# Performance work log

Measured on AMD Instinct MI355X. Metric: run time of the kernel, lower is better.

The kernel has to match this reference:

```python
import jax, jax.numpy as jnp
import numpy as np

N_NODES = 50000


def _graph_conv(x, edges, W0, b0, W1, b1):
    # Symmetric (undirected) message passing: each edge (a,b) sends x[b]->a and x[a]->b.
    src = jnp.concatenate([edges[:, 0], edges[:, 1]])  # [2E]
    dst = jnp.concatenate([edges[:, 1], edges[:, 0]])  # [2E]
    deg = jax.ops.segment_sum(jnp.ones_like(dst, dtype=x.dtype), dst, num_segments=N_NODES)
    deg = jnp.maximum(deg, 1.0)  # avoid div-by-zero for isolated nodes
    agg = jax.ops.segment_sum(x[src], dst, num_segments=N_NODES) / deg[:, None]  # [N, F]
    # self transform + normalized-neighbor transform
    return x @ W0 + b0 + agg @ W1 + b1


def setup_inputs() -> dict:
    key = jax.random.key(0)
    ks = jax.random.split(key, 10)
    feats = [256, 512, 256]  # [in] + hidden + [out]
    inp = {
        "vert_features": jax.random.normal(ks[0], (N_NODES, feats[0]), dtype=jnp.float32),
        "edges": jax.random.randint(ks[1], (400000, 2), 0, N_NODES, dtype=jnp.int64),
    }
    kidx = 2
    for l, (fi, fo) in enumerate(zip(feats[:-1], feats[1:])):
        s = 1.0 / np.sqrt(fi)
        inp[f"W0_{l}"] = jax.random.normal(ks[kidx], (fi, fo), dtype=jnp.float32) * s
        inp[f"b0_{l}"] = jnp.zeros((fo,), dtype=jnp.float32)
        inp[f"W1_{l}"] = jax.random.normal(ks[kidx + 1], (fi, fo), dtype=jnp.float32) * s
        inp[f"b1_{l}"] = jnp.zeros((fo,), dtype=jnp.float32)
        kidx += 2
    return inp


def reference(vert_features, edges, W0_0, b0_0, W1_0, b1_0, W0_1, b0_1, W1_1, b1_1):
    # layer 0 + ReLU
    x = _graph_conv(vert_features, edges, W0_0, b0_0, W1_0, b1_0)
    x = jax.nn.relu(x)
    # final layer (no activation)
    x = _graph_conv(x, edges, W0_1, b0_1, W1_1, b1_1)
    return x
```

## Files before the change

### kernel.cpp

```cpp
#include <hip/hip_runtime.h>
#include <stdint.h>

typedef __bf16  bf16x8 __attribute__((ext_vector_type(8)));
typedef float   f32x4  __attribute__((ext_vector_type(4)));

__device__ __forceinline__ unsigned short f2bf(float f) {
  unsigned int u = __float_as_uint(f);
  u += 0x7fffu + ((u >> 16) & 1u);
  return (unsigned short)(u >> 16);
}
__device__ __forceinline__ float bflo(unsigned int v) { return __uint_as_float(v << 16); }
__device__ __forceinline__ float bfhi(unsigned int v) { return __uint_as_float(v & 0xffff0000u); }

__global__ void detect_fmt_kernel(const int* __restrict__ eg, int* __restrict__ fmt) {
  if (threadIdx.x == 0 && blockIdx.x == 0) {
    int is64 = 1;
    for (int i = 1; i < 32; i += 2) if (eg[i] != 0) { is64 = 0; break; }
    fmt[0] = is64;
  }
}

__global__ void phase1_kernel(const float* __restrict__ x, unsigned short* __restrict__ A0, int n,
                              const int* __restrict__ eg, const int* __restrict__ fmt,
                              int* __restrict__ deg, int E,
                              const float* __restrict__ W00, const float* __restrict__ W10,
                              const float* __restrict__ W01, const float* __restrict__ W11,
                              const float* __restrict__ b00, const float* __restrict__ b10,
                              const float* __restrict__ b01, const float* __restrict__ b11,
                              unsigned short* __restrict__ Bt1, unsigned short* __restrict__ Bt2,
                              float* __restrict__ bias1, float* __restrict__ bias2) {
  const int i = blockIdx.x * 256 + threadIdx.x;
  if (i < n * 64) {
    const int row = i >> 6, c4 = i & 63;
    const float4 v = ((const float4*)x)[i];
    ushort4 o;
    o.x = f2bf(v.x); o.y = f2bf(v.y); o.z = f2bf(v.z); o.w = f2bf(v.w);
    *(ushort4*)&A0[(size_t)row * 512 + c4 * 4] = o;
  }
  if (i < 512 * 512) {
    const int nn = i >> 9, k = i & 511;
    const float v1 = (k < 256) ? W00[k * 512 + nn] : W10[(k - 256) * 512 + nn];
    Bt1[i] = f2bf(v1);
    const float v2 = (nn < 256) ? W01[k * 256 + nn] : W11[k * 256 + (nn - 256)];
    Bt2[i] = f2bf(v2);
    if (i < 512) {
      bias1[i] = b00[i] + b10[i];
      bias2[i] = (i < 256) ? (b01[i] + b11[i]) : 0.f;
    }
  }
  if (i < E) {
    int a, b;
    if (fmt[0]) { a = eg[4 * i]; b = eg[4 * i + 2]; }
    else        { a = eg[2 * i]; b = eg[2 * i + 1]; }
    if ((unsigned)a < (unsigned)n && (unsigned)b < (unsigned)n) {
      atomicAdd(&deg[a], 1);
      atomicAdd(&deg[b], 1);
    }
  }
}

__global__ void block_sum_kernel(const int* __restrict__ deg, int* __restrict__ bsum, int n) {
  const int t = threadIdx.x;
  const int i = blockIdx.x * 1024 + t;
  int v = (i < n) ? deg[i] : 0;
  #pragma unroll
  for (int d = 32; d > 0; d >>= 1) v += __shfl_xor(v, d);
  __shared__ int ws[16];
  if ((t & 63) == 0) ws[t >> 6] = v;
  __syncthreads();
  if (t < 16) {
    int s = ws[t];
    #pragma unroll
    for (int d = 1; d < 16; d <<= 1) s += __shfl_xor(s, d);
    if (t == 0) bsum[blockIdx.x] = s;
  }
}

__global__ void scan_bsum_kernel(int* __restrict__ bsum, int* __restrict__ off, int nb, int n) {
  const int l = threadIdx.x;
  int v = (l < nb) ? bsum[l] : 0;
  const int orig = v;
  #pragma unroll
  for (int d = 1; d < 64; d <<= 1) {
    int u = __shfl_up(v, d);
    if (l >= d) v += u;
  }
  if (l < nb) bsum[l] = v - orig;
  if (l == nb - 1) off[n] = v;
}

__global__ void scan_final_kernel(const int* __restrict__ deg, const int* __restrict__ bsum,
                                  int* __restrict__ off, float* __restrict__ invd, int n) {
  const int t = threadIdx.x;
  const int i = blockIdx.x * 1024 + t;
  const int lane = t & 63, wid = t >> 6;
  const int v = (i < n) ? deg[i] : 0;
  int s = v;
  #pragma unroll
  for (int d = 1; d < 64; d <<= 1) {
    int u = __shfl_up(s, d);
    if (lane >= d) s += u;
  }
  __shared__ int ws[16];
  if (lane == 63) ws[wid] = s;
  __syncthreads();
  if (t < 16) {
    int w = ws[t];
    #pragma unroll
    for (int d = 1; d < 16; d <<= 1) {
      int u = __shfl_up(w, d);
      if (t >= d) w += u;
    }
    ws[t] = w;
  }
  __syncthreads();
  const int add = (wid > 0) ? ws[wid - 1] : 0;
  const int incl = s + add;
  if (i < n) {
    off[i] = bsum[blockIdx.x] + incl - v;
    invd[i] = 1.f / (float)(v > 1 ? v : 1);
  }
}

__global__ void fill_kernel(const int* __restrict__ eg, const int* __restrict__ fmt,
                            const int* __restrict__ off, int* __restrict__ cur,
                            int* __restrict__ adj, int E, int n) {
  const int e = blockIdx.x * 256 + threadIdx.x;
  if (e >= E) return;
  int a, b;
  if (fmt[0]) { a = eg[4 * e]; b = eg[4 * e + 2]; }
  else        { a = eg[2 * e]; b = eg[2 * e + 1]; }
  if ((unsigned)a >= (unsigned)n || (unsigned)b >= (unsigned)n) return;
  int p = atomicAdd(&cur[b], 1); adj[off[b] + p] = a;
  int q = atomicAdd(&cur[a], 1); adj[off[a] + q] = b;
}

__global__ __launch_bounds__(256) void agg_gather0_kernel(
    const unsigned short* A0r, unsigned short* A0w,
    const int* __restrict__ adj, const int* __restrict__ off,
    const float* __restrict__ invd, int n) {
  const int node = blockIdx.x * 4 + (threadIdx.x >> 6);
  const int lane = threadIdx.x & 63;
  if (node >= n) return;
  const int s = off[node], e = off[node + 1];
  float a0 = 0.f, a1 = 0.f, a2 = 0.f, a3 = 0.f;
  for (int base = s; base < e; base += 64) {
    const int cnt = min(64, e - base);
    const int idxv = (lane < cnt) ? adj[base + lane] : 0;
    int j = 0;
    for (; j + 4 <= cnt; j += 4) {
      const int p0 = __shfl(idxv, j), p1 = __shfl(idxv, j + 1);
      const int p2 = __shfl(idxv, j + 2), p3 = __shfl(idxv, j + 3);
      const uint2 v0 = *(const uint2*)&A0r[(size_t)p0 * 512 + lane * 4];
      const uint2 v1 = *(const uint2*)&A0r[(size_t)p1 * 512 + lane * 4];
      const uint2 v2 = *(const uint2*)&A0r[(size_t)p2 * 512 + lane * 4];
      const uint2 v3 = *(const uint2*)&A0r[(size_t)p3 * 512 + lane * 4];
      a0 += bflo(v0.x) + bflo(v1.x) + bflo(v2.x) + bflo(v3.x);
      a1 += bfhi(v0.x) + bfhi(v1.x) + bfhi(v2.x) + bfhi(v3.x);
      a2 += bflo(v0.y) + bflo(v1.y) + bflo(v2.y) + bflo(v3.y);
      a3 += bfhi(v0.y) + bfhi(v1.y) + bfhi(v2.y) + bfhi(v3.y);
    }
    for (; j < cnt; ++j) {
      const int nbr = __shfl(idxv, j);
      const uint2 v = *(const uint2*)&A0r[(size_t)nbr * 512 + lane * 4];
      a0 += bflo(v.x); a1 += bfhi(v.x);
      a2 += bflo(v.y); a3 += bfhi(v.y);
    }
  }
  const float sc = invd[node];
  ushort4 o;
  o.x = f2bf(a0 * sc); o.y = f2bf(a1 * sc); o.z = f2bf(a2 * sc); o.w = f2bf(a3 * sc);
  *(ushort4*)&A0w[(size_t)node * 512 + 256 + lane * 4] = o;
}

__global__ __launch_bounds__(256) void agg_out_kernel(
    const unsigned short* __restrict__ Z, float* out,
    const int* __restrict__ adj, const int* __restrict__ off,
    const float* __restrict__ invd, int n) {
  const int node = blockIdx.x * 4 + (threadIdx.x >> 6);
  const int lane = threadIdx.x & 63;
  if (node >= n) return;
  const int s = off[node], e = off[node + 1];
  float a0 = 0.f, a1 = 0.f, a2 = 0.f, a3 = 0.f;
  for (int base = s; base < e; base += 64) {
    const int cnt = min(64, e - base);
    const int idxv = (lane < cnt) ? adj[base + lane] : 0;
    int j = 0;
    for (; j + 4 <= cnt; j += 4) {
      const int p0 = __shfl(idxv, j), p1 = __shfl(idxv, j + 1);
      const int p2 = __shfl(idxv, j + 2), p3 = __shfl(idxv, j + 3);
      const uint2 v0 = *(const uint2*)&Z[(size_t)p0 * 256 + lane * 4];
      const uint2 v1 = *(const uint2*)&Z[(size_t)p1 * 256 + lane * 4];
      const uint2 v2 = *(const uint2*)&Z[(size_t)p2 * 256 + lane * 4];
      const uint2 v3 = *(const uint2*)&Z[(size_t)p3 * 256 + lane * 4];
      a0 += bflo(v0.x) + bflo(v1.x) + bflo(v2.x) + bflo(v3.x);
      a1 += bfhi(v0.x) + bfhi(v1.x) + bfhi(v2.x) + bfhi(v3.x);
      a2 += bflo(v0.y) + bflo(v1.y) + bflo(v2.y) + bflo(v3.y);
      a3 += bfhi(v0.y) + bfhi(v1.y) + bfhi(v2.y) + bfhi(v3.y);
    }
    for (; j < cnt; ++j) {
      const int nbr = __shfl(idxv, j);
      const uint2 v = *(const uint2*)&Z[(size_t)nbr * 256 + lane * 4];
      a0 += bflo(v.x); a1 += bfhi(v.x);
      a2 += bflo(v.y); a3 += bfhi(v.y);
    }
  }
  const float sc = invd[node];
  float4* po = (float4*)&out[(size_t)node * 256 + lane * 4];
  float4 o = *po;
  o.x += sc * a0; o.y += sc * a1; o.z += sc * a2; o.w += sc * a3;
  *po = o;
}

template<int MODE>
__global__ __launch_bounds__(256, 4) void gemm_kernel(
    const unsigned short* __restrict__ A, const unsigned short* __restrict__ Bt,
    const float* __restrict__ bias,
    unsigned short* __restrict__ Hout, float* __restrict__ Pout, unsigned short* __restrict__ Zout,
    int M_real, int nwg) {
  constexpr int K = 512;
  constexpr int BK = 32;
  __shared__ unsigned short sm[4][128 * BK];
  const int t = threadIdx.x;
  const int lane = t & 63;
  const int wid = t >> 6;
  const int wr = wid >> 1;
  const int wc = wid & 1;

  const int orig = blockIdx.x;
  const int q = nwg >> 3, r = nwg & 7;
  const int xcd = orig & 7, bidx = orig >> 3;
  const int wgid = (xcd < r ? xcd * (q + 1) : r * (q + 1) + (xcd - r) * q) + bidx;
  const int m0 = (wgid >> 2) * 128;
  const int n0 = (wgid & 3) * 128;

  f32x4 acc[4][4];
  #pragma unroll
  for (int m = 0; m < 4; ++m)
    #pragma unroll
    for (int n = 0; n < 4; ++n)
      acc[m][n] = f32x4{0.f, 0.f, 0.f, 0.f};

  auto stage = [&](int buf, int kt) {
    #pragma unroll
    for (int i = 0; i < 2; ++i) {
      const int row = i * 64 + (t >> 2);
      const int c = (t & 3) ^ ((row >> 1) & 3);
      const unsigned short* ga = A + (size_t)(m0 + row) * K + kt * BK + c * 8;
      __builtin_amdgcn_global_load_lds(
          (const __attribute__((address_space(1))) unsigned int*)ga,
          (__attribute__((address_space(3))) unsigned int*)&sm[buf][(i * 256 + t) * 8], 16, 0, 0);
    }
    #pragma unroll
    for (int i = 0; i < 2; ++i) {
      const int row = i * 64 + (t >> 2);
      const int c = (t & 3) ^ ((row >> 1) & 3);
      const unsigned short* gb = Bt + (size_t)(n0 + row) * K + kt * BK + c * 8;
      __builtin_amdgcn_global_load_lds(
          (const __attribute__((address_space(1))) unsigned int*)gb,
          (__attribute__((address_space(3))) unsigned int*)&sm[2 + buf][(i * 256 + t) * 8], 16, 0, 0);
    }
  };

  auto compute = [&](int buf) {
    bf16x8 aF[4], bF[4];
    #pragma unroll
    for (int m = 0; m < 4; ++m) {
      const int row = wr * 64 + m * 16 + (lane & 15);
      const int sl = (lane >> 4) ^ ((row >> 1) & 3);
      aF[m] = *(const bf16x8*)&sm[buf][row * BK + sl * 8];
    }
    #pragma unroll
    for (int n = 0; n < 4; ++n) {
      const int row = wc * 64 + n * 16 + (lane & 15);
      const int sl = (lane >> 4) ^ ((row >> 1) & 3);
      bF[n] = *(const bf16x8*)&sm[2 + buf][row * BK + sl * 8];
    }
    #pragma unroll
    for (int m = 0; m < 4; ++m)
      #pragma unroll
      for (int n = 0; n < 4; ++n)
        acc[m][n] = __builtin_amdgcn_mfma_f32_16x16x32_bf16(aF[m], bF[n], acc[m][n], 0, 0, 0);
  };

  stage(0, 0);
  __syncthreads();
  int cur = 0;
  #pragma unroll 1
  for (int kt = 0; kt < K / BK - 1; ++kt) {
    stage(cur ^ 1, kt + 1);
    compute(cur);
    __syncthreads();
    cur ^= 1;
  }
  compute(cur);
  __syncthreads();

  if (MODE == 0 || n0 >= 256) {
    unsigned short* ep = &sm[0][0];
    #pragma unroll
    for (int n = 0; n < 4; ++n) {
      const int lcol = wc * 64 + n * 16 + (lane & 15);
      const float bc = (MODE == 0) ? bias[n0 + lcol] : 0.f;
      #pragma unroll
      for (int m = 0; m < 4; ++m) {
        #pragma unroll
        for (int rr = 0; rr < 4; ++rr) {
          const int lr = wr * 64 + m * 16 + (lane >> 4) * 4 + rr;
          float y = acc[m][n][rr] + bc;
          if (MODE == 0) y = y > 0.f ? y : 0.f;
          ep[lr * 128 + (lcol ^ (((lr >> 2) & 7) << 4))] = f2bf(y);
        }
      }
    }
    __syncthreads();
    unsigned short* dst = (MODE == 0) ? Hout : Zout;
    const int ld = (MODE == 0) ? 512 : 256;
    const int cb0 = (MODE == 0) ? n0 : (n0 - 256);
    #pragma unroll
    for (int p = 0; p < 8; ++p) {
      const int tr = p * 16 + (t >> 4);
      const int cb = (t & 15) * 8;
      const uint4 v = *(const uint4*)&ep[tr * 128 + (cb ^ (((tr >> 2) & 7) << 4))];
      *(uint4*)&dst[(size_t)(m0 + tr) * ld + cb0 + cb] = v;
    }
  } else {
    float* ep = (float*)&sm[0][0];
    #pragma unroll
    for (int pp = 0; pp < 2; ++pp) {
      if (wr == pp) {
        #pragma unroll
        for (int n = 0; n < 4; ++n) {
          const int lcol = wc * 64 + n * 16 + (lane & 15);
          const float bc = bias[n0 + lcol];
          #pragma unroll
          for (int m = 0; m < 4; ++m)
            #pragma unroll
            for (int rr = 0; rr < 4; ++rr) {
              const int lr = m * 16 + (lane >> 4) * 4 + rr;
              ep[lr * 128 + (lcol ^ (((lr >> 2) & 7) << 4))] = acc[m][n][rr] + bc;
            }
        }
      }
      __syncthreads();
      const int tr = t >> 2;
      const int grow = m0 + pp * 64 + tr;
      if (grow < M_real) {
        #pragma unroll
        for (int j = 0; j < 8; ++j) {
          const int cb = (t & 3) * 32 + j * 4;
          const float4 v = *(const float4*)&ep[tr * 128 + (cb ^ (((tr >> 2) & 7) << 4))];
          *(float4*)&Pout[(size_t)grow * 256 + n0 + cb] = v;
        }
      }
      __syncthreads();
    }
  }
}

extern "C" void kernel_launch(void* const* d_in, const int* in_sizes, int n_in,
                              void* d_out, int out_size, void* d_ws, size_t ws_size,
                              hipStream_t stream) {
  const float* x   = (const float*)d_in[0];
  const int* edges = (const int*)d_in[1];
  const float* W00 = (const float*)d_in[2];
  const float* b00 = (const float*)d_in[3];
  const float* W10 = (const float*)d_in[4];
  const float* b10 = (const float*)d_in[5];
  const float* W01 = (const float*)d_in[6];
  const float* b01 = (const float*)d_in[7];
  const float* W11 = (const float*)d_in[8];
  const float* b11 = (const float*)d_in[9];
  float* out = (float*)d_out;

  const int n = in_sizes[0] / 256;
  const int E = in_sizes[1] / 2;
  const int Mpad = ((n + 127) / 128) * 128;

  char* p = (char*)d_ws;
  auto alloc = [&](size_t bytes) { char* r = p; p += (bytes + 255) & ~(size_t)255; return r; };
  unsigned short* A0   = (unsigned short*)alloc((size_t)Mpad * 512 * 2);
  unsigned short* H    = (unsigned short*)alloc((size_t)Mpad * 512 * 2);
  unsigned short* Z    = (unsigned short*)alloc((size_t)Mpad * 256 * 2);
  unsigned short* Bt1  = (unsigned short*)alloc(512 * 512 * 2);
  unsigned short* Bt2  = (unsigned short*)alloc(512 * 512 * 2);
  float* bias1 = (float*)alloc(512 * 4);
  float* bias2 = (float*)alloc(512 * 4);
  int*   deg   = (int*)alloc((size_t)n * 4);
  int*   curp  = (int*)alloc((size_t)n * 4);
  int*   off   = (int*)alloc((size_t)(n + 1) * 4);
  int*   bsum  = (int*)alloc(256 * 4);
  float* invd  = (float*)alloc((size_t)n * 4);
  int*   adj   = (int*)alloc((size_t)2 * E * 4);
  int*   fmt   = (int*)alloc(256);

  hipMemsetAsync(deg,  0, (size_t)n * 4, stream);
  hipMemsetAsync(curp, 0, (size_t)n * 4, stream);

  detect_fmt_kernel<<<1, 64, 0, stream>>>(edges, fmt);

  const int p1_blocks = (n * 64 + 255) / 256;
  phase1_kernel<<<p1_blocks, 256, 0, stream>>>(x, A0, n, edges, fmt, deg, E,
                                               W00, W10, W01, W11, b00, b10, b01, b11,
                                               Bt1, Bt2, bias1, bias2);

  const int nb = (n + 1023) / 1024;
  block_sum_kernel<<<nb, 1024, 0, stream>>>(deg, bsum, n);
  scan_bsum_kernel<<<1, 64, 0, stream>>>(bsum, off, nb, n);
  scan_final_kernel<<<nb, 1024, 0, stream>>>(deg, bsum, off, invd, n);
  fill_kernel<<<(E + 255) / 256, 256, 0, stream>>>(edges, fmt, off, curp, adj, E, n);

  agg_gather0_kernel<<<(n + 3) / 4, 256, 0, stream>>>(A0, A0, adj, off, invd, n);

  const int nwg = (Mpad / 128) * 4;
  gemm_kernel<0><<<nwg, 256, 0, stream>>>(A0, Bt1, bias1, H, nullptr, nullptr, n, nwg);
  gemm_kernel<1><<<nwg, 256, 0, stream>>>(H, Bt2, bias2, nullptr, out, Z, n, nwg);

  agg_out_kernel<<<(n + 3) / 4, 256, 0, stream>>>(Z, out, adj, off, invd, n);
}
```

Baseline: 321.3 us.

## Slice neighbor aggregation by feature columns with 8 neighbors per wave

Both aggregation kernels now split each node's 256 feature columns into 8 slices across separate blocks. Each wave processes 8 neighbors at a time, with 8 lanes reading 32 contiguous columns per neighbor, then reduces across lane groups with xor shuffles. This raises memory-level parallelism and occupancy for the gather, in exchange for 8x more blocks, repeated reads of the adjacency list, and shorter 64-byte row segments per load. Zeroing of the cursor array also moves from a memset into the scan kernel, dropping one launch.

```diff
diff --git a/kernel.cpp b/kernel.cpp
--- a/kernel.cpp
+++ b/kernel.cpp
@@ -90,7 +90,8 @@
 }
 
 __global__ void scan_final_kernel(const int* __restrict__ deg, const int* __restrict__ bsum,
-                                  int* __restrict__ off, float* __restrict__ invd, int n) {
+                                  int* __restrict__ off, float* __restrict__ invd,
+                                  int* __restrict__ curp, int n) {
   const int t = threadIdx.x;
   const int i = blockIdx.x * 1024 + t;
   const int lane = t & 63, wid = t >> 6;
@@ -119,6 +120,7 @@
   if (i < n) {
     off[i] = bsum[blockIdx.x] + incl - v;
     invd[i] = 1.f / (float)(v > 1 ? v : 1);
+    curp[i] = 0;
   }
 }
 
@@ -135,81 +137,102 @@
   int q = atomicAdd(&cur[a], 1); adj[off[a] + q] = b;
 }
 
-__global__ __launch_bounds__(256) void agg_gather0_kernel(
+
+__global__ __launch_bounds__(256) void agg0_sliced_kernel(
     const unsigned short* A0r, unsigned short* A0w,
     const int* __restrict__ adj, const int* __restrict__ off,
     const float* __restrict__ invd, int n) {
-  const int node = blockIdx.x * 4 + (threadIdx.x >> 6);
+  const int slice = blockIdx.x & 7;
+  const int node = (blockIdx.x >> 3) * 4 + (threadIdx.x >> 6);
+  if (node >= n) return;
   const int lane = threadIdx.x & 63;
-  if (node >= n) return;
+  const int grp = lane >> 3;
+  const int c0 = slice * 32 + (lane & 7) * 4;
   const int s = off[node], e = off[node + 1];
   float a0 = 0.f, a1 = 0.f, a2 = 0.f, a3 = 0.f;
   for (int base = s; base < e; base += 64) {
     const int cnt = min(64, e - base);
     const int idxv = (lane < cnt) ? adj[base + lane] : 0;
+    const int jmax = (cnt + 7) >> 3;
     int j = 0;
-    for (; j + 4 <= cnt; j += 4) {
-      const int p0 = __shfl(idxv, j), p1 = __shfl(idxv, j + 1);
-      const int p2 = __shfl(idxv, j + 2), p3 = __shfl(idxv, j + 3);
-      const uint2 v0 = *(const uint2*)&A0r[(size_t)p0 * 512 + lane * 4];
-      const uint2 v1 = *(const uint2*)&A0r[(size_t)p1 * 512 + lane * 4];
-      const uint2 v2 = *(const uint2*)&A0r[(size_t)p2 * 512 + lane * 4];
-      const uint2 v3 = *(const uint2*)&A0r[(size_t)p3 * 512 + lane * 4];
-      a0 += bflo(v0.x) + bflo(v1.x) + bflo(v2.x) + bflo(v3.x);
-      a1 += bfhi(v0.x) + bfhi(v1.x) + bfhi(v2.x) + bfhi(v3.x);
-      a2 += bflo(v0.y) + bflo(v1.y) + bflo(v2.y) + bflo(v3.y);
-      a3 += bfhi(v0.y) + bfhi(v1.y) + bfhi(v2.y) + bfhi(v3.y);
-    }
-    for (; j < cnt; ++j) {
-      const int nbr = __shfl(idxv, j);
-      const uint2 v = *(const uint2*)&A0r[(size_t)nbr * 512 + lane * 4];
-      a0 += bflo(v.x); a1 += bfhi(v.x);
-      a2 += bflo(v.y); a3 += bfhi(v.y);
-    }
-  }
-  const float sc = invd[node];
-  ushort4 o;
-  o.x = f2bf(a0 * sc); o.y = f2bf(a1 * sc); o.z = f2bf(a2 * sc); o.w = f2bf(a3 * sc);
-  *(ushort4*)&A0w[(size_t)node * 512 + 256 + lane * 4] = o;
-}
-
-__global__ __launch_bounds__(256) void agg_out_kernel(
+    for (; j + 2 <= jmax; j += 2) {
+      const int s0 = j * 8 + grp, s1 = s0 + 8;
+      const int p0 = __shfl(idxv, s0), p1 = __shfl(idxv, s1);
+      uint2 v0 = make_uint2(0u, 0u), v1 = make_uint2(0u, 0u);
+      if (s0 < cnt) v0 = *(const uint2*)&A0r[(size_t)p0 * 512 + c0];
+      if (s1 < cnt) v1 = *(const uint2*)&A0r[(size_t)p1 * 512 + c0];
+      a0 += bflo(v0.x) + bflo(v1.x); a1 += bfhi(v0.x) + bfhi(v1.x);
+      a2 += bflo(v0.y) + bflo(v1.y); a3 += bfhi(v0.y) + bfhi(v1.y);
+    }
+    for (; j < jmax; ++j) {
+      const int s0 = j * 8 + grp;
+      const int p0 = __shfl(idxv, s0);
+      uint2 v0 = make_uint2(0u, 0u);
+      if (s0 < cnt) v0 = *(const uint2*)&A0r[(size_t)p0 * 512 + c0];
+      a0 += bflo(v0.x); a1 += bfhi(v0.x);
+      a2 += bflo(v0.y); a3 += bfhi(v0.y);
+    }
+  }
+  #pragma unroll
+  for (int d = 8; d < 64; d <<= 1) {
+    a0 += __shfl_xor(a0, d); a1 += __shfl_xor(a1, d);
+    a2 += __shfl_xor(a2, d); a3 += __shfl_xor(a3, d);
+  }
+  if (grp == 0) {
+    const float sc = invd[node];
+    ushort4 o;
+    o.x = f2bf(a0 * sc); o.y = f2bf(a1 * sc); o.z = f2bf(a2 * sc); o.w = f2bf(a3 * sc);
+    *(ushort4*)&A0w[(size_t)node * 512 + 256 + c0] = o;
+  }
+}
+
+__global__ __launch_bounds__(256) void agg_out_sliced_kernel(
     const unsigned short* __restrict__ Z, float* out,
     const int* __restrict__ adj, const int* __restrict__ off,
     const float* __restrict__ invd, int n) {
-  const int node = blockIdx.x * 4 + (threadIdx.x >> 6);
+  const int slice = blockIdx.x & 7;
+  const int node = (blockIdx.x >> 3) * 4 + (threadIdx.x >> 6);
+  if (node >= n) return;
   const int lane = threadIdx.x & 63;
-  if (node >= n) return;
+  const int grp = lane >> 3;
+  const int c0 = slice * 32 + (lane & 7) * 4;
   const int s = off[node], e = off[node + 1];
   float a0 = 0.f, a1 = 0.f, a2 = 0.f, a3 = 0.f;
   for (int base = s; base < e; base += 64) {
     const int cnt = min(64, e - base);
     const int idxv = (lane < cnt) ? adj[base + lane] : 0;
+    const int jmax = (cnt + 7) >> 3;
     int j = 0;
-    for (; j + 4 <= cnt; j += 4) {
-      const int p0 = __shfl(idxv, j), p1 = __shfl(idxv, j + 1);
-      const int p2 = __shfl(idxv, j + 2), p3 = __shfl(idxv, j + 3);
-      const uint2 v0 = *(const uint2*)&Z[(size_t)p0 * 256 + lane * 4];
-      const uint2 v1 = *(const uint2*)&Z[(size_t)p1 * 256 + lane * 4];
-      const uint2 v2 = *(const uint2*)&Z[(size_t)p2 * 256 + lane * 4];
-      const uint2 v3 = *(const uint2*)&Z[(size_t)p3 * 256 + lane * 4];
-      a0 += bflo(v0.x) + bflo(v1.x) + bflo(v2.x) + bflo(v3.x);
-      a1 += bfhi(v0.x) + bfhi(v1.x) + bfhi(v2.x) + bfhi(v3.x);
-      a2 += bflo(v0.y) + bflo(v1.y) + bflo(v2.y) + bflo(v3.y);
-      a3 += bfhi(v0.y) + bfhi(v1.y) + bfhi(v2.y) + bfhi(v3.y);
-    }
-    for (; j < cnt; ++j) {
-      const int nbr = __shfl(idxv, j);
-      const uint2 v = *(const uint2*)&Z[(size_t)nbr * 256 + lane * 4];
-      a0 += bflo(v.x); a1 += bfhi(v.x);
-      a2 += bflo(v.y); a3 += bfhi(v.y);
-    }
-  }
-  const float sc = invd[node];
-  float4* po = (float4*)&out[(size_t)node * 256 + lane * 4];
-  float4 o = *po;
-  o.x += sc * a0; o.y += sc * a1; o.z += sc * a2; o.w += sc * a3;
-  *po = o;
+    for (; j + 2 <= jmax; j += 2) {
+      const int s0 = j * 8 + grp, s1 = s0 + 8;
+      const int p0 = __shfl(idxv, s0), p1 = __shfl(idxv, s1);
+      uint2 v0 = make_uint2(0u, 0u), v1 = make_uint2(0u, 0u);
+      if (s0 < cnt) v0 = *(const uint2*)&Z[(size_t)p0 * 256 + c0];
+      if (s1 < cnt) v1 = *(const uint2*)&Z[(size_t)p1 * 256 + c0];
+      a0 += bflo(v0.x) + bflo(v1.x); a1 += bfhi(v0.x) + bfhi(v1.x);
+      a2 += bflo(v0.y) + bflo(v1.y); a3 += bfhi(v0.y) + bfhi(v1.y);
+    }
+    for (; j < jmax; ++j) {
+      const int s0 = j * 8 + grp;
+      const int p0 = __shfl(idxv, s0);
+      uint2 v0 = make_uint2(0u, 0u);
+      if (s0 < cnt) v0 = *(const uint2*)&Z[(size_t)p0 * 256 + c0];
+      a0 += bflo(v0.x); a1 += bfhi(v0.x);
+      a2 += bflo(v0.y); a3 += bfhi(v0.y);
+    }
+  }
+  #pragma unroll
+  for (int d = 8; d < 64; d <<= 1) {
+    a0 += __shfl_xor(a0, d); a1 += __shfl_xor(a1, d);
+    a2 += __shfl_xor(a2, d); a3 += __shfl_xor(a3, d);
+  }
+  if (grp == 0) {
+    const float sc = invd[node];
+    float4* po = (float4*)&out[(size_t)node * 256 + c0];
+    float4 o = *po;
+    o.x += sc * a0; o.y += sc * a1; o.z += sc * a2; o.w += sc * a3;
+    *po = o;
+  }
 }
 
 template<int MODE>
@@ -394,8 +417,7 @@
   int*   adj   = (int*)alloc((size_t)2 * E * 4);
   int*   fmt   = (int*)alloc(256);
 
-  hipMemsetAsync(deg,  0, (size_t)n * 4, stream);
-  hipMemsetAsync(curp, 0, (size_t)n * 4, stream);
+  hipMemsetAsync(deg, 0, (size_t)n * 4, stream);
 
   detect_fmt_kernel<<<1, 64, 0, stream>>>(edges, fmt);
 
@@ -407,14 +429,15 @@
   const int nb = (n + 1023) / 1024;
   block_sum_kernel<<<nb, 1024, 0, stream>>>(deg, bsum, n);
   scan_bsum_kernel<<<1, 64, 0, stream>>>(bsum, off, nb, n);
-  scan_final_kernel<<<nb, 1024, 0, stream>>>(deg, bsum, off, invd, n);
+  scan_final_kernel<<<nb, 1024, 0, stream>>>(deg, bsum, off, invd, curp, n);
   fill_kernel<<<(E + 255) / 256, 256, 0, stream>>>(edges, fmt, off, curp, adj, E, n);
 
-  agg_gather0_kernel<<<(n + 3) / 4, 256, 0, stream>>>(A0, A0, adj, off, invd, n);
+  const int agg_blocks = 8 * ((n + 3) / 4);
+  agg0_sliced_kernel<<<agg_blocks, 256, 0, stream>>>(A0, A0, adj, off, invd, n);
 
   const int nwg = (Mpad / 128) * 4;
   gemm_kernel<0><<<nwg, 256, 0, stream>>>(A0, Bt1, bias1, H, nullptr, nullptr, n, nwg);
   gemm_kernel<1><<<nwg, 256, 0, stream>>>(H, Bt2, bias2, nullptr, out, Z, n, nwg);
 
-  agg_out_kernel<<<(n + 3) / 4, 256, 0, stream>>>(Z, out, adj, off, invd, n);
-}
+  agg_out_sliced_kernel<<<agg_blocks, 256, 0, stream>>>(Z, out, adj, off, invd, n);
+}
```

After: 452.4 us. 1.41x slower.
